# Kernel tuning notes

Hardware: AMD Instinct MI355X
Metric: run time of the kernel (lower is better)

Reference implementation:

```python
import jax, jax.numpy as jnp
import numpy as np

B, T, H, IN, OUT, FUT = 256, 512, 512, 1, 1, 16


def setup_inputs() -> dict:
    key = jax.random.key(0)
    ks = jax.random.split(key, 11)
    bound = 1.0 / np.sqrt(H)  # torch LSTMCell/Linear default init
    u = lambda kk, sh: jax.random.uniform(kk, sh, jnp.float32, -bound, bound)
    fbias = lambda b: b.at[H:2 * H].set(1.0)  # forget-gate bias filled with 1.0 per __init__
    return {
        "x": jax.random.normal(ks[0], (B, T), jnp.float32),
        "Wih0": u(ks[1], (4 * H, IN)),
        "Whh0": u(ks[2], (4 * H, H)),
        "bih0": fbias(u(ks[3], (4 * H,))),
        "bhh0": fbias(u(ks[4], (4 * H,))),
        "Wih1": u(ks[5], (4 * H, H)),
        "Whh1": u(ks[6], (4 * H, H)),
        "bih1": fbias(u(ks[7], (4 * H,))),
        "bhh1": fbias(u(ks[8], (4 * H,))),
        "Wlin": u(ks[9], (OUT, H)),
        "blin": u(ks[10], (OUT,)),
        "future": FUT,
    }


def _cell(xv, h, c, Wih, Whh, bih, bhh):
    # torch.nn.LSTMCell: gates ordered (i, f, g, o)
    gates = xv @ Wih.T + h @ Whh.T + bih + bhh
    i, f, g, o = jnp.split(gates, 4, axis=-1)
    c = jax.nn.sigmoid(f) * c + jax.nn.sigmoid(i) * jnp.tanh(g)
    h = jax.nn.sigmoid(o) * jnp.tanh(c)
    return h, c


def reference(x, Wih0, Whh0, bih0, bhh0, Wih1, Whh1, bih1, bhh1, Wlin, blin, future):
    params = ((Wih0, Whh0, bih0, bhh0), (Wih1, Whh1, bih1, bhh1))
    Bsz, hid = x.shape[0], Whh0.shape[1]
    h0 = tuple(jnp.zeros((Bsz, hid), x.dtype) for _ in params)
    c0 = tuple(jnp.zeros((Bsz, hid), x.dtype) for _ in params)

    def layer_stack(inp, hs, cs):
        new_h, new_c = [], []
        for j, (Wih, Whh, bih, bhh) in enumerate(params):
            h, c = _cell(inp, hs[j], cs[j], Wih, Whh, bih, bhh)
            new_h.append(h)
            new_c.append(c)
            inp = h
        return tuple(new_h), tuple(new_c), inp

    def cond_step(carry, xt):  # xt: [B, 1]
        hs, cs = carry
        hs, cs, top = layer_stack(xt, hs, cs)
        out = top @ Wlin.T + blin  # [B, 1]
        return (hs, cs), out

    xs = jnp.swapaxes(x, 0, 1)[:, :, None]  # [T, B, 1]
    (hs, cs), outs = jax.lax.scan(cond_step, (h0, c0), xs)
    last = outs[-1]

    def fut_step(carry, _):
        hs, cs, out = carry
        hs, cs, top = layer_stack(out, hs, cs)
        out = top @ Wlin.T + blin
        return (hs, cs, out), out

    _, fut_outs = jax.lax.scan(fut_step, (hs, cs, last), None, length=future)

    all_outs = jnp.concatenate([outs, fut_outs], axis=0)  # [T+future, B, 1]
    return jnp.swapaxes(all_outs, 0, 1)[:, :, 0]  # [B, T+future]
```

## Files before the change

### kernel.cpp

```cpp
#include <hip/hip_runtime.h>
#include <hip/hip_bf16.h>
#include <math.h>

#define HID    512
#define BATCH  256
#define TLEN   512
#define FUT    16
#define NSTEP  (TLEN + FUT)
#define NGRP   16
#define WPG    16
#define BPG    16
#define UPW    32
#define NR     128

#define OFF_W0   0u
#define OFF_W1   2097152u
#define OFF_CA   6291456u
#define OFF_XF   7340032u
#define OFF_WI   7357440u
#define OFF_B0   7365632u
#define OFF_B1   7373824u
#define OFF_BAR  7382016u
#define OFF_XT   7384064u

typedef __bf16 bf16x8 __attribute__((ext_vector_type(8)));
typedef float  f32x4  __attribute__((ext_vector_type(4)));

__device__ __forceinline__ float sigf(float v)      { return 1.f / (1.f + __expf(-v)); }
__device__ __forceinline__ float tanh_fast(float v) { return 2.f / (1.f + __expf(-2.f * v)) - 1.f; }

__device__ __forceinline__ void store_short_llc(void* p, unsigned short v) {
    asm volatile("global_store_short %0, %1, off sc0 sc1"
                 :: "v"(p), "v"((unsigned)v) : "memory");
}

__device__ __forceinline__ void gl2lds16_llc(const void* g, void* l) {
    __builtin_amdgcn_global_load_lds(
        (const __attribute__((address_space(1))) void*)g,
        (__attribute__((address_space(3))) void*)l, 16, 0, 17);
}

__device__ __forceinline__ void flag_barrier(unsigned* flags, int m, unsigned phase) {
    __builtin_amdgcn_s_waitcnt(0);
    __syncthreads();
    if (threadIdx.x == 0)
        __hip_atomic_store(&flags[m], phase, __ATOMIC_RELAXED, __HIP_MEMORY_SCOPE_AGENT);
    if (threadIdx.x < 64) {
        const int lane = threadIdx.x;
        for (;;) {
            unsigned f = phase;
            if (lane < WPG)
                f = __hip_atomic_load(&flags[lane], __ATOMIC_RELAXED, __HIP_MEMORY_SCOPE_AGENT);
            if (__ballot(f >= phase) == ~0ull) break;
            __builtin_amdgcn_s_sleep(1);
        }
    }
    __syncthreads();
}

__global__ void lstm_init(char* __restrict__ ws, float* __restrict__ out,
                          const float* __restrict__ blin)
{
    float bl = blin[0];
    int tid = blockIdx.x * blockDim.x + threadIdx.x;
    int stride = gridDim.x * blockDim.x;
    uint4* ca = (uint4*)(ws + OFF_CA);
    for (int i = tid; i < 65536; i += stride) ca[i] = make_uint4(0u, 0u, 0u, 0u);
    float* xf = (float*)(ws + OFF_XF);
    for (int i = tid; i < (FUT + 1) * BATCH; i += stride) xf[i] = bl;
    unsigned* bar = (unsigned*)(ws + OFF_BAR);
    for (int i = tid; i < NGRP * 32; i += stride) bar[i] = 0u;
    for (int i = tid; i < BATCH * NSTEP; i += stride) out[i] = bl;
}

__global__ void lstm_pack(char* __restrict__ ws,
    const float* __restrict__ x,
    const float* __restrict__ Wih0, const float* __restrict__ Whh0,
    const float* __restrict__ bih0, const float* __restrict__ bhh0,
    const float* __restrict__ Wih1, const float* __restrict__ Whh1,
    const float* __restrict__ bih1, const float* __restrict__ bhh1)
{
    int tid = blockIdx.x * blockDim.x + threadIdx.x;
    int stride = gridDim.x * blockDim.x;

    __hip_bfloat16* W0p = (__hip_bfloat16*)(ws + OFF_W0);
    for (int i = tid; i < 16 * 128 * 512; i += stride) {
        int k = i & 511, r = (i >> 9) & 127, m = i >> 16;
        int row = (r >> 5) * HID + m * UPW + (r & 31);
        W0p[i] = __float2bfloat16(Whh0[(size_t)row * HID + k]);
    }
    __hip_bfloat16* W1p = (__hip_bfloat16*)(ws + OFF_W1);
    for (int i = tid; i < 16 * 128 * 1024; i += stride) {
        int k = i & 1023, r = (i >> 10) & 127, m = i >> 17;
        int row = (r >> 5) * HID + m * UPW + (r & 31);
        float v = (k < 512) ? Wih1[(size_t)row * HID + k] : Whh1[(size_t)row * HID + (k - 512)];
        W1p[i] = __float2bfloat16(v);
    }
    float* wi = (float*)(ws + OFF_WI);
    float* b0 = (float*)(ws + OFF_B0);
    float* b1 = (float*)(ws + OFF_B1);
    for (int i = tid; i < 16 * 128; i += stride) {
        int r = i & 127, m = i >> 7;
        int row = (r >> 5) * HID + m * UPW + (r & 31);
        wi[i] = Wih0[row];
        b0[i] = bih0[row] + bhh0[row];
        b1[i] = bih1[row] + bhh1[row];
    }
    float* xT = (float*)(ws + OFF_XT);
    for (int i = tid; i < TLEN * BATCH; i += stride) {
        int t = i >> 8, b = i & 255;
        xT[i] = x[(size_t)b * TLEN + t];
    }
}

__global__ __launch_bounds__(512, 2) void lstm_persist(
    const float* __restrict__ wlin,
    float* __restrict__ out, char* __restrict__ ws)
{
    const int tid  = threadIdx.x;
    const int lane = tid & 63;
    const int wave = tid >> 6;
    const int g    = blockIdx.x & 15;
    const int m    = blockIdx.x >> 4;
    const int bbase = g * BPG;

    __shared__ __attribute__((aligned(16))) __hip_bfloat16 As[16 * 1024];
    __shared__ float g0S[16][136];
    __shared__ float g1S[16][136];
    char* AsB = (char*)As;

    {
        int* az = (int*)As;
        for (int i = tid; i < (16 * 1024 * 2) / 4; i += 512) az[i] = 0;
    }

    const float* wis = (const float*)(ws + OFF_WI) + m * NR;
    const float* b0s = (const float*)(ws + OFF_B0) + m * NR;
    const float* b1s = (const float*)(ws + OFF_B1) + m * NR;
    char* CAg = ws + OFF_CA + (size_t)g * 65536;
    float* xfeed = (float*)(ws + OFF_XF);
    const float* xT = (const float*)(ws + OFF_XT);
    unsigned* flags = (unsigned*)(ws + OFF_BAR) + g * 32;

    const int fl = lane & 15;
    const int fq = lane >> 4;
    const int w  = wave;
    const int us  = tid & 31;
    const int b0r = tid >> 5;

    const float wl0 = wlin[m * UPW + us];
    float wiR[4], b0R[4], b1R[4];
#pragma unroll
    for (int q = 0; q < 4; ++q) {
        wiR[q] = wis[q * 32 + us];
        b0R[q] = b0s[q * 32 + us];
        b1R[q] = b1s[q * 32 + us];
    }
    float c00 = 0.f, c10 = 0.f;

    const int cgr  = 4 * m + (us >> 3);
    const int pub0 = b0r * 1024 + (((cgr + b0r) & 63) << 4) + (us & 7) * 2;

    const bf16x8* W0row = (const bf16x8*)(ws + OFF_W0 + (size_t)m * NR * 512 * 2)
                          + (size_t)(w * 16 + fl) * 64;
    const bf16x8* W1row = (const bf16x8*)(ws + OFF_W1 + (size_t)m * NR * 1024 * 2)
                          + (size_t)(w * 16 + fl) * 128;
    bf16x8 w0f[16], w1f[32];
#pragma unroll
    for (int ks = 0; ks < 16; ++ks) w0f[ks] = W0row[ks * 4 + fq];
#pragma unroll
    for (int ks = 0; ks < 32; ++ks) w1f[ks] = W1row[ks * 4 + fq];

    __syncthreads();

    const bf16x8* Asv = (const bf16x8*)As;

    unsigned phase = 0;
    for (int t = 0; t < NSTEP; ++t) {
        const int p = t & 1;
        char* CAp = CAg + p * 32768;
        char* CAq = CAg + (1 - p) * 32768;

        float xv0;
        if (t < TLEN) {
            xv0 = xT[t * BATCH + bbase + b0r];
        } else {
            xv0 = xfeed[(t - TLEN) * BATCH + bbase + b0r];
        }

        f32x4 acc0 = {0.f, 0.f, 0.f, 0.f};
#pragma unroll
        for (int ks = 0; ks < 16; ++ks) {
            int c = ks * 4 + fq;
            bf16x8 a0 = Asv[fl * 128 + ((c + fl) & 63)];
            acc0 = __builtin_amdgcn_mfma_f32_16x16x32_bf16(a0, w0f[ks], acc0, 0, 0, 0);
        }
#pragma unroll
        for (int i = 0; i < 4; ++i)
            g0S[fq * 4 + i][w * 16 + fl] = acc0[i];
        __syncthreads();

        {
            float gi = g0S[b0r][us]      + b0R[0] + xv0 * wiR[0];
            float gf = g0S[b0r][32 + us] + b0R[1] + xv0 * wiR[1];
            float gg = g0S[b0r][64 + us] + b0R[2] + xv0 * wiR[2];
            float go = g0S[b0r][96 + us] + b0R[3] + xv0 * wiR[3];
            c00 = sigf(gf) * c00 + sigf(gi) * tanh_fast(gg);
            __hip_bfloat16 h = __float2bfloat16(sigf(go) * tanh_fast(c00));
            store_short_llc(CAp + pub0, *(unsigned short*)&h);
        }

        ++phase;
        flag_barrier(flags, m, phase);

        {
#pragma unroll
            for (int ci = 0; ci < 2; ++ci) {
                int b = wave * 2 + ci;
                gl2lds16_llc(CAp + b * 1024 + lane * 16,
                             AsB + b * 2048 + lane * 16);
                gl2lds16_llc(CAq + 16384 + b * 1024 + lane * 16,
                             AsB + b * 2048 + 1024 + lane * 16);
            }
            __builtin_amdgcn_s_waitcnt(0);
            __syncthreads();
        }

        acc0 = (f32x4){0.f, 0.f, 0.f, 0.f};
#pragma unroll
        for (int ks = 0; ks < 16; ++ks) {
            int c = ks * 4 + fq;
            bf16x8 a0 = Asv[fl * 128 + ((c + fl) & 63)];
            acc0 = __builtin_amdgcn_mfma_f32_16x16x32_bf16(a0, w1f[ks], acc0, 0, 0, 0);
        }
#pragma unroll
        for (int ks = 16; ks < 32; ++ks) {
            int c = (ks - 16) * 4 + fq;
            bf16x8 a0 = Asv[fl * 128 + 64 + ((c + fl) & 63)];
            acc0 = __builtin_amdgcn_mfma_f32_16x16x32_bf16(a0, w1f[ks], acc0, 0, 0, 0);
        }
#pragma unroll
        for (int i = 0; i < 4; ++i)
            g1S[fq * 4 + i][w * 16 + fl] = acc0[i];
        __syncthreads();

        {
            float gi = g1S[b0r][us]      + b1R[0];
            float gf = g1S[b0r][32 + us] + b1R[1];
            float gg = g1S[b0r][64 + us] + b1R[2];
            float go = g1S[b0r][96 + us] + b1R[3];
            c10 = sigf(gf) * c10 + sigf(gi) * tanh_fast(gg);
            float h = sigf(go) * tanh_fast(c10);
            __hip_bfloat16 hb = __float2bfloat16(h);
            store_short_llc(CAp + 16384 + pub0, *(unsigned short*)&hb);
            float po = wl0 * h;
#pragma unroll
            for (int off = 1; off < 32; off <<= 1) po += __shfl_xor(po, off, 64);
            if (us == 0) {
                atomicAdd(&out[(size_t)(bbase + b0r) * NSTEP + t], po);
                if (t >= TLEN - 1)
                    atomicAdd(&xfeed[(t - (TLEN - 1)) * BATCH + bbase + b0r], po);
            }
        }

        if (t >= TLEN - 1) {
            ++phase;
            flag_barrier(flags, m, phase);
        }
    }
}

extern "C" void kernel_launch(void* const* d_in, const int* in_sizes, int n_in,
                              void* d_out, int out_size, void* d_ws, size_t ws_size,
                              hipStream_t stream)
{
    const float* x    = (const float*)d_in[0];
    const float* Wih0 = (const float*)d_in[1];
    const float* Whh0 = (const float*)d_in[2];
    const float* bih0 = (const float*)d_in[3];
    const float* bhh0 = (const float*)d_in[4];
    const float* Wih1 = (const float*)d_in[5];
    const float* Whh1 = (const float*)d_in[6];
    const float* bih1 = (const float*)d_in[7];
    const float* bhh1 = (const float*)d_in[8];
    const float* Wlin = (const float*)d_in[9];
    const float* blin = (const float*)d_in[10];
    float* out = (float*)d_out;
    char* ws = (char*)d_ws;

    hipLaunchKernelGGL(lstm_init, dim3(256), dim3(256), 0, stream, ws, out, blin);
    hipLaunchKernelGGL(lstm_pack, dim3(512), dim3(256), 0, stream,
                       ws, x, Wih0, Whh0, bih0, bhh0, Wih1, Whh1, bih1, bhh1);
    hipLaunchKernelGGL(lstm_persist, dim3(256), dim3(512), 0, stream, Wlin, out, ws);
}
```

Baseline: 2.365 ms.

## Skew layer pipeline so both layers' matmuls share one barrier per step

Restructures the time loop as a software pipeline. Layer 0 of step t and layer 1 of step t-1 are computed together, so each conditioned step needs one cross-block flag barrier instead of two syncthreads-separated phases. The layer-1 pointwise update runs at the start of the next iteration, and a final epilogue finishes the last step. During the future phase, feedback still forces an extra barrier per step, and the skewed ordering adds complexity around the double-buffered hidden-state indices.

```diff
diff --git a/kernel.cpp b/kernel.cpp
--- a/kernel.cpp
+++ b/kernel.cpp
@@ -132,6 +132,8 @@
     {
         int* az = (int*)As;
         for (int i = tid; i < (16 * 1024 * 2) / 4; i += 512) az[i] = 0;
+        float* gz = &g0S[0][0];
+        for (int i = tid; i < 16 * 136; i += 512) gz[i] = 0.f;
     }
 
     const float* wis = (const float*)(ws + OFF_WI) + m * NR;
@@ -181,33 +183,62 @@
         char* CAp = CAg + p * 32768;
         char* CAq = CAg + (1 - p) * 32768;
 
-        float xv0;
-        if (t < TLEN) {
-            xv0 = xT[t * BATCH + bbase + b0r];
+        if (t >= TLEN) {
+            {
+                float gi = g1S[b0r][us]      + b1R[0];
+                float gf = g1S[b0r][32 + us] + b1R[1];
+                float gg = g1S[b0r][64 + us] + b1R[2];
+                float go = g1S[b0r][96 + us] + b1R[3];
+                c10 = sigf(gf) * c10 + sigf(gi) * tanh_fast(gg);
+                float h = sigf(go) * tanh_fast(c10);
+                __hip_bfloat16 hb = __float2bfloat16(h);
+                store_short_llc(CAq + 16384 + pub0, *(unsigned short*)&hb);
+                float po = wl0 * h;
+#pragma unroll
+                for (int off = 1; off < 32; off <<= 1) po += __shfl_xor(po, off, 64);
+                if (us == 0) {
+                    atomicAdd(&out[(size_t)(bbase + b0r) * NSTEP + (t - 1)], po);
+                    atomicAdd(&xfeed[(t - TLEN) * BATCH + bbase + b0r], po);
+                }
+            }
+            ++phase;
+            flag_barrier(flags, m, phase);
+            {
+                float xv0 = xfeed[(t - TLEN) * BATCH + bbase + b0r];
+                float gi = g0S[b0r][us]      + b0R[0] + xv0 * wiR[0];
+                float gf = g0S[b0r][32 + us] + b0R[1] + xv0 * wiR[1];
+                float gg = g0S[b0r][64 + us] + b0R[2] + xv0 * wiR[2];
+                float go = g0S[b0r][96 + us] + b0R[3] + xv0 * wiR[3];
+                c00 = sigf(gf) * c00 + sigf(gi) * tanh_fast(gg);
+                __hip_bfloat16 h = __float2bfloat16(sigf(go) * tanh_fast(c00));
+                store_short_llc(CAp + pub0, *(unsigned short*)&h);
+            }
         } else {
-            xv0 = xfeed[(t - TLEN) * BATCH + bbase + b0r];
-        }
-
-        f32x4 acc0 = {0.f, 0.f, 0.f, 0.f};
-#pragma unroll
-        for (int ks = 0; ks < 16; ++ks) {
-            int c = ks * 4 + fq;
-            bf16x8 a0 = Asv[fl * 128 + ((c + fl) & 63)];
-            acc0 = __builtin_amdgcn_mfma_f32_16x16x32_bf16(a0, w0f[ks], acc0, 0, 0, 0);
-        }
-#pragma unroll
-        for (int i = 0; i < 4; ++i)
-            g0S[fq * 4 + i][w * 16 + fl] = acc0[i];
-        __syncthreads();
-
-        {
-            float gi = g0S[b0r][us]      + b0R[0] + xv0 * wiR[0];
-            float gf = g0S[b0r][32 + us] + b0R[1] + xv0 * wiR[1];
-            float gg = g0S[b0r][64 + us] + b0R[2] + xv0 * wiR[2];
-            float go = g0S[b0r][96 + us] + b0R[3] + xv0 * wiR[3];
-            c00 = sigf(gf) * c00 + sigf(gi) * tanh_fast(gg);
-            __hip_bfloat16 h = __float2bfloat16(sigf(go) * tanh_fast(c00));
-            store_short_llc(CAp + pub0, *(unsigned short*)&h);
+            {
+                float xv0 = xT[t * BATCH + bbase + b0r];
+                float gi = g0S[b0r][us]      + b0R[0] + xv0 * wiR[0];
+                float gf = g0S[b0r][32 + us] + b0R[1] + xv0 * wiR[1];
+                float gg = g0S[b0r][64 + us] + b0R[2] + xv0 * wiR[2];
+                float go = g0S[b0r][96 + us] + b0R[3] + xv0 * wiR[3];
+                c00 = sigf(gf) * c00 + sigf(gi) * tanh_fast(gg);
+                __hip_bfloat16 h = __float2bfloat16(sigf(go) * tanh_fast(c00));
+                store_short_llc(CAp + pub0, *(unsigned short*)&h);
+            }
+            if (t > 0) {
+                float gi = g1S[b0r][us]      + b1R[0];
+                float gf = g1S[b0r][32 + us] + b1R[1];
+                float gg = g1S[b0r][64 + us] + b1R[2];
+                float go = g1S[b0r][96 + us] + b1R[3];
+                c10 = sigf(gf) * c10 + sigf(gi) * tanh_fast(gg);
+                float h = sigf(go) * tanh_fast(c10);
+                __hip_bfloat16 hb = __float2bfloat16(h);
+                store_short_llc(CAq + 16384 + pub0, *(unsigned short*)&hb);
+                float po = wl0 * h;
+#pragma unroll
+                for (int off = 1; off < 32; off <<= 1) po += __shfl_xor(po, off, 64);
+                if (us == 0)
+                    atomicAdd(&out[(size_t)(bbase + b0r) * NSTEP + (t - 1)], po);
+            }
         }
 
         ++phase;
@@ -226,47 +257,51 @@
             __syncthreads();
         }
 
-        acc0 = (f32x4){0.f, 0.f, 0.f, 0.f};
-#pragma unroll
-        for (int ks = 0; ks < 16; ++ks) {
-            int c = ks * 4 + fq;
-            bf16x8 a0 = Asv[fl * 128 + ((c + fl) & 63)];
-            acc0 = __builtin_amdgcn_mfma_f32_16x16x32_bf16(a0, w1f[ks], acc0, 0, 0, 0);
-        }
-#pragma unroll
-        for (int ks = 16; ks < 32; ++ks) {
-            int c = (ks - 16) * 4 + fq;
-            bf16x8 a0 = Asv[fl * 128 + 64 + ((c + fl) & 63)];
-            acc0 = __builtin_amdgcn_mfma_f32_16x16x32_bf16(a0, w1f[ks], acc0, 0, 0, 0);
-        }
-#pragma unroll
-        for (int i = 0; i < 4; ++i)
-            g1S[fq * 4 + i][w * 16 + fl] = acc0[i];
+        {
+            f32x4 acc = {0.f, 0.f, 0.f, 0.f};
+#pragma unroll
+            for (int ks = 0; ks < 16; ++ks) {
+                int c = ks * 4 + fq;
+                bf16x8 a0 = Asv[fl * 128 + ((c + fl) & 63)];
+                acc = __builtin_amdgcn_mfma_f32_16x16x32_bf16(a0, w0f[ks], acc, 0, 0, 0);
+            }
+#pragma unroll
+            for (int i = 0; i < 4; ++i)
+                g0S[fq * 4 + i][w * 16 + fl] = acc[i];
+        }
+        {
+            f32x4 acc = {0.f, 0.f, 0.f, 0.f};
+#pragma unroll
+            for (int ks = 0; ks < 16; ++ks) {
+                int c = ks * 4 + fq;
+                bf16x8 a0 = Asv[fl * 128 + ((c + fl) & 63)];
+                acc = __builtin_amdgcn_mfma_f32_16x16x32_bf16(a0, w1f[ks], acc, 0, 0, 0);
+            }
+#pragma unroll
+            for (int ks = 16; ks < 32; ++ks) {
+                int c = (ks - 16) * 4 + fq;
+                bf16x8 a0 = Asv[fl * 128 + 64 + ((c + fl) & 63)];
+                acc = __builtin_amdgcn_mfma_f32_16x16x32_bf16(a0, w1f[ks], acc, 0, 0, 0);
+            }
+#pragma unroll
+            for (int i = 0; i < 4; ++i)
+                g1S[fq * 4 + i][w * 16 + fl] = acc[i];
+        }
         __syncthreads();
-
-        {
-            float gi = g1S[b0r][us]      + b1R[0];
-            float gf = g1S[b0r][32 + us] + b1R[1];
-            float gg = g1S[b0r][64 + us] + b1R[2];
-            float go = g1S[b0r][96 + us] + b1R[3];
-            c10 = sigf(gf) * c10 + sigf(gi) * tanh_fast(gg);
-            float h = sigf(go) * tanh_fast(c10);
-            __hip_bfloat16 hb = __float2bfloat16(h);
-            store_short_llc(CAp + 16384 + pub0, *(unsigned short*)&hb);
-            float po = wl0 * h;
-#pragma unroll
-            for (int off = 1; off < 32; off <<= 1) po += __shfl_xor(po, off, 64);
-            if (us == 0) {
-                atomicAdd(&out[(size_t)(bbase + b0r) * NSTEP + t], po);
-                if (t >= TLEN - 1)
-                    atomicAdd(&xfeed[(t - (TLEN - 1)) * BATCH + bbase + b0r], po);
-            }
-        }
-
-        if (t >= TLEN - 1) {
-            ++phase;
-            flag_barrier(flags, m, phase);
-        }
+    }
+
+    {
+        float gi = g1S[b0r][us]      + b1R[0];
+        float gf = g1S[b0r][32 + us] + b1R[1];
+        float gg = g1S[b0r][64 + us] + b1R[2];
+        float go = g1S[b0r][96 + us] + b1R[3];
+        c10 = sigf(gf) * c10 + sigf(gi) * tanh_fast(gg);
+        float h = sigf(go) * tanh_fast(c10);
+        float po = wl0 * h;
+#pragma unroll
+        for (int off = 1; off < 32; off <<= 1) po += __shfl_xor(po, off, 64);
+        if (us == 0)
+            atomicAdd(&out[(size_t)(bbase + b0r) * NSTEP + (NSTEP - 1)], po);
     }
 }
 
```

Result: slower. 2.808 ms (+18.7%).
